# Kernel tuning notes

Hardware: AMD Instinct MI355X
Metric: run time of the kernel (lower is better)

The kernel has to match this reference:

```python
import jax, jax.numpy as jnp
import numpy as np

DIM = 128          # per-stream channels (init arg `dim`)
C = 2 * DIM        # fused channels
NH = 8             # num_heads
HD = C // NH       # head_dim = 32
K = 3              # kernel_size
DIL = (2, 3)       # dilation list
ND = len(DIL)
SCALE = HD ** -0.5


def setup_inputs() -> dict:
    key = jax.random.key(0)
    ks = jax.random.split(key, 4)
    B, H, W = 4, 80, 80
    rgb = jax.random.normal(ks[0], (B, DIM, H, W), jnp.float32)
    ir = jax.random.normal(ks[1], (B, DIM, H, W), jnp.float32)
    w_qkv = jax.random.normal(ks[2], (3 * C, C), jnp.float32) * (C ** -0.5)
    w_proj = jax.random.normal(ks[3], (C, C), jnp.float32) * (C ** -0.5)
    b_proj = jnp.zeros((C,), jnp.float32)
    return {"rgb": rgb, "ir": ir, "w_qkv": w_qkv, "w_proj": w_proj, "b_proj": b_proj}


def _unfold(x, k, d):
    # nn.Unfold(k, dilation=d, padding=d*(k-1)//2, stride=1) -> [B, c, k*k, H, W]
    B, c, H, W = x.shape
    p = d * (k - 1) // 2
    xp = jnp.pad(x, ((0, 0), (0, 0), (p, p), (p, p)))
    pats = [xp[:, :, i * d:i * d + H, j * d:j * d + W]
            for i in range(k) for j in range(k)]
    return jnp.stack(pats, axis=2)


def _dilate_attention(q, k, v, d):
    # q,k,v: [B, c, H, W] with c = C // ND; attention over k*k dilated neighborhood
    B, c, H, W = q.shape
    h = c // HD
    N = H * W
    qr = q.reshape(B, h, HD, N)                      # [B,h,hd,N]
    ku = _unfold(k, K, d).reshape(B, h, HD, K * K, N)  # [B,h,hd,K2,N]
    vu = _unfold(v, K, d).reshape(B, h, HD, K * K, N)
    attn = jnp.einsum('bhdn,bhdkn->bhnk', qr, ku) * SCALE   # [B,h,N,K2]
    attn = jax.nn.softmax(attn, axis=-1)
    out = jnp.einsum('bhnk,bhdkn->bnhd', attn, vu)          # head-major channels
    return out.reshape(B, H, W, c)


def reference(rgb, ir, w_qkv, w_proj, b_proj):
    y = jnp.concatenate([rgb, ir], axis=1)            # [B, C, H, W]
    B, Cc, H, W = y.shape
    # 1x1 conv qkv, then split channels as [3, num_dilation, C//num_dilation]
    qkv = jnp.einsum('bchw,oc->bohw', y, w_qkv).reshape(B, 3, ND, Cc // ND, H, W)
    outs = [_dilate_attention(qkv[:, 0, i], qkv[:, 1, i], qkv[:, 2, i], DIL[i])
            for i in range(ND)]
    x = jnp.concatenate(outs, axis=-1)                # [B, H, W, C], dilation-major
    x = x @ w_proj.T + b_proj                         # proj Linear(C, C)
    # residual: add rgb to first half of channels, ir to second half
    return x + y.transpose(0, 2, 3, 1)
```

## Files before the change

### kernel.cpp

```cpp
#include <hip/hip_runtime.h>

#define HH 80
#define WW 80
#define NPIX 6400
#define NB 4
#define BN 25600
#define CDIM 256
#define QKVC 768
#define SCALE 0.17677669529663689f

typedef __attribute__((ext_vector_type(8))) short short8;
typedef __attribute__((ext_vector_type(4))) float floatx4;

__device__ __forceinline__ float b2f(ushort u) {
    return __uint_as_float(((uint)u) << 16);
}
__device__ __forceinline__ ushort f2b(float f) {
    uint u = __float_as_uint(f);
    return (ushort)((u + 0x7fffu + ((u >> 16) & 1u)) >> 16);
}
__device__ __forceinline__ void unpack8(uint4 v, float* f) {
    f[0] = __uint_as_float(v.x << 16); f[1] = __uint_as_float(v.x & 0xffff0000u);
    f[2] = __uint_as_float(v.y << 16); f[3] = __uint_as_float(v.y & 0xffff0000u);
    f[4] = __uint_as_float(v.z << 16); f[5] = __uint_as_float(v.z & 0xffff0000u);
    f[6] = __uint_as_float(v.w << 16); f[7] = __uint_as_float(v.w & 0xffff0000u);
}
__device__ __forceinline__ void gload_lds16(const void* gptr, void* lptr) {
    __builtin_amdgcn_global_load_lds(
        (const __attribute__((address_space(1))) unsigned int*)gptr,
        (__attribute__((address_space(3))) unsigned int*)lptr,
        16, 0, 0);
}

__global__ __launch_bounds__(256) void cast_all_k(
    const float* __restrict__ rgb, const float* __restrict__ ir,
    const float* __restrict__ wq, const float* __restrict__ wp,
    ushort* __restrict__ Yb, ushort* __restrict__ wqb, ushort* __restrict__ wpb)
{
    const int tid = threadIdx.x;
    if (blockIdx.x >= 100) {
        int i = (((blockIdx.x - 100) * 8 + blockIdx.y) * 4 + blockIdx.z) * 256 + tid;
        if (i < QKVC * CDIM) wqb[i] = f2b(wq[i]);
        else                 wpb[i - QKVC * CDIM] = f2b(wp[i - QKVC * CDIM]);
        return;
    }
    __shared__ ushort T[32][72];
    const int pix0 = blockIdx.x * 64;
    const int cb = blockIdx.y;
    const int b = blockIdx.z;

    const int pl = tid & 63, cg = tid >> 6;
    #pragma unroll
    for (int cc = 0; cc < 32; cc += 4) {
        int c = cb * 32 + cc + cg;
        const float* src = (c < 128) ? (rgb + ((size_t)b * 128 + c) * NPIX)
                                     : (ir + ((size_t)b * 128 + (c - 128)) * NPIX);
        T[cc + cg][pl] = f2b(src[pix0 + pl]);
    }
    __syncthreads();
    const int nl = tid >> 2, c0 = (tid & 3) * 8;
    ushort tmp[8];
    #pragma unroll
    for (int j = 0; j < 8; ++j) tmp[j] = T[c0 + j][nl];
    uint4 v;
    v.x = tmp[0] | ((uint)tmp[1] << 16);
    v.y = tmp[2] | ((uint)tmp[3] << 16);
    v.z = tmp[4] | ((uint)tmp[5] << 16);
    v.w = tmp[6] | ((uint)tmp[7] << 16);
    *(uint4*)(&Yb[((size_t)(b * NPIX + pix0 + nl)) * CDIM + cb * 32 + c0]) = v;
}

__device__ __forceinline__ void gemm_nt_body(
    const ushort* __restrict__ A, const ushort* __restrict__ W,
    ushort* As, ushort* Bs, int n0, int o0, floatx4 acc[4][4])
{
    const int tid = threadIdx.x;
    const int lane = tid & 63;
    const int wave = tid >> 6;
    const int wr = wave >> 1, wc = wave & 1;
    const int l15 = lane & 15, quad = lane >> 4;

    const int srow = tid >> 2;
    const int sk   = (tid & 3) * 8;

    for (int k0 = 0; k0 < CDIM; k0 += 32) {
        #pragma unroll
        for (int p = 0; p < 2; ++p) {
            gload_lds16(&A[(size_t)(n0 + p * 64 + srow) * CDIM + k0 + sk],
                        As + wave * 512 + p * 2048);
            gload_lds16(&W[(size_t)(o0 + p * 64 + srow) * CDIM + k0 + sk],
                        Bs + wave * 512 + p * 2048);
        }
        __syncthreads();
        short8 af[4], bfr[4];
        #pragma unroll
        for (int i = 0; i < 4; ++i)
            af[i] = *(const short8*)(&As[(wr * 64 + i * 16 + l15) * 32 + quad * 8]);
        #pragma unroll
        for (int j = 0; j < 4; ++j)
            bfr[j] = *(const short8*)(&Bs[(wc * 64 + j * 16 + l15) * 32 + quad * 8]);
        #pragma unroll
        for (int i = 0; i < 4; ++i)
            #pragma unroll
            for (int j = 0; j < 4; ++j)
                acc[i][j] = __builtin_amdgcn_mfma_f32_16x16x32_bf16(
                    af[i], bfr[j], acc[i][j], 0, 0, 0);
        __syncthreads();
    }
}

__global__ __launch_bounds__(256) void gemm_qkv_mfma(
    const ushort* __restrict__ Yb, const ushort* __restrict__ Wb,
    ushort* __restrict__ qkv2)
{
    __shared__ __align__(16) ushort As[128 * 32];
    __shared__ __align__(16) ushort Bs[128 * 32];
    const int tid = threadIdx.x;
    const int lane = tid & 63;
    const int wave = tid >> 6;
    const int wr = wave >> 1, wc = wave & 1;
    const int l15 = lane & 15, quad = lane >> 4;
    const int n0 = blockIdx.x * 128;
    const int o0 = blockIdx.y * 128;

    floatx4 acc[4][4] = {};
    gemm_nt_body(Yb, Wb, As, Bs, n0, o0, acc);

    #pragma unroll
    for (int i = 0; i < 4; ++i)
        #pragma unroll
        for (int j = 0; j < 4; ++j) {
            const int o = o0 + wc * 64 + j * 16 + l15;
            ushort* cbase = qkv2 + (size_t)(o >> 5) * BN * 32 + (o & 31);
            #pragma unroll
            for (int r = 0; r < 4; ++r) {
                int n = n0 + wr * 64 + i * 16 + quad * 4 + r;
                cbase[(size_t)n * 32] = f2b(acc[i][j][r]);
            }
        }
}

template<int D>
__device__ __forceinline__ void attn_tile(
    const ushort* __restrict__ qkv2, ushort* __restrict__ X2,
    ushort* kl, int b, int dh, int y0, int x0)
{
    constexpr int RW = 16 + 2 * D;
    constexpr int RP = RW * RW;
    const int tid = threadIdx.x;
    const int lane = tid & 63;
    const int wave = tid >> 6;
    const ushort* Qc = qkv2 + (size_t)dh * BN * 32;
    const ushort* Kc = qkv2 + (size_t)(8 + dh) * BN * 32;
    const ushort* Vc = qkv2 + (size_t)(16 + dh) * BN * 32;

    const int px = tid & 15, py = tid >> 4;
    const int n = b * NPIX + (y0 + py) * WW + (x0 + px);
    float q[32];
    {
        const uint4* qp = (const uint4*)(Qc + (size_t)n * 32);
        uint4 v0 = qp[0], v1 = qp[1], v2 = qp[2], v3 = qp[3];
        unpack8(v0, q); unpack8(v1, q + 8); unpack8(v2, q + 16); unpack8(v3, q + 24);
    }

    for (int p0 = 0; p0 < RP; p0 += 64) {
        int p = p0 + lane;
        int ry = p / RW, rx = p % RW;
        int gy = min(max(y0 - D + ry, 0), HH - 1);
        int gx = min(max(x0 - D + rx, 0), WW - 1);
        if (p < RP)
            gload_lds16(Kc + (size_t)(b * NPIX + gy * WW + gx) * 32 + wave * 8,
                        kl + (size_t)(wave * RP + p0) * 8);
    }
    __syncthreads();

    float sc[9];
    #pragma unroll
    for (int t = 0; t < 9; ++t) {
        const int dy = t / 3 - 1, dx = t % 3 - 1;
        const int yy = y0 + py + dy * D, xx = x0 + px + dx * D;
        const int p = (py + D + dy * D) * RW + (px + D + dx * D);
        float s = 0.f;
        if (yy >= 0 && yy < HH && xx >= 0 && xx < WW) {
            #pragma unroll
            for (int c = 0; c < 4; ++c) {
                float kv[8];
                unpack8(*(const uint4*)(kl + (size_t)(c * RP + p) * 8), kv);
                #pragma unroll
                for (int j = 0; j < 8; ++j) s += q[c * 8 + j] * kv[j];
            }
        }
        sc[t] = s * SCALE;
    }
    float m = sc[0];
    #pragma unroll
    for (int t = 1; t < 9; ++t) m = fmaxf(m, sc[t]);
    float sum = 0.f;
    #pragma unroll
    for (int t = 0; t < 9; ++t) { sc[t] = __expf(sc[t] - m); sum += sc[t]; }
    const float inv = 1.f / sum;

    __syncthreads();
    for (int p0 = 0; p0 < RP; p0 += 64) {
        int p = p0 + lane;
        int ry = p / RW, rx = p % RW;
        int gy = min(max(y0 - D + ry, 0), HH - 1);
        int gx = min(max(x0 - D + rx, 0), WW - 1);
        if (p < RP)
            gload_lds16(Vc + (size_t)(b * NPIX + gy * WW + gx) * 32 + wave * 8,
                        kl + (size_t)(wave * RP + p0) * 8);
    }
    __syncthreads();

    float o[32];
    #pragma unroll
    for (int hd = 0; hd < 32; ++hd) o[hd] = 0.f;
    #pragma unroll
    for (int t = 0; t < 9; ++t) {
        const int dy = t / 3 - 1, dx = t % 3 - 1;
        const int yy = y0 + py + dy * D, xx = x0 + px + dx * D;
        const int p = (py + D + dy * D) * RW + (px + D + dx * D);
        if (yy >= 0 && yy < HH && xx >= 0 && xx < WW) {
            const float wgt = sc[t] * inv;
            #pragma unroll
            for (int c = 0; c < 4; ++c) {
                float vv[8];
                unpack8(*(const uint4*)(kl + (size_t)(c * RP + p) * 8), vv);
                #pragma unroll
                for (int j = 0; j < 8; ++j) o[c * 8 + j] += wgt * vv[j];
            }
        }
    }
    uint4* xp = (uint4*)(X2 + (size_t)dh * BN * 32 + (size_t)n * 32);
    #pragma unroll
    for (int m4 = 0; m4 < 4; ++m4) {
        uint4 v;
        v.x = f2b(o[8 * m4 + 0]) | ((uint)f2b(o[8 * m4 + 1]) << 16);
        v.y = f2b(o[8 * m4 + 2]) | ((uint)f2b(o[8 * m4 + 3]) << 16);
        v.z = f2b(o[8 * m4 + 4]) | ((uint)f2b(o[8 * m4 + 5]) << 16);
        v.w = f2b(o[8 * m4 + 6]) | ((uint)f2b(o[8 * m4 + 7]) << 16);
        xp[m4] = v;
    }
}

__global__ __launch_bounds__(256) void attn2_k(
    const ushort* __restrict__ qkv2, ushort* __restrict__ X2)
{
    __shared__ __align__(16) ushort kl[4 * 484 * 8];
    const int tile = blockIdx.x;
    const int y0 = (tile / 5) * 16, x0 = (tile % 5) * 16;
    const int dh = blockIdx.y;
    const int b = blockIdx.z;
    if (dh < 4) attn_tile<2>(qkv2, X2, kl, b, dh, y0, x0);
    else        attn_tile<3>(qkv2, X2, kl, b, dh, y0, x0);
}

__global__ __launch_bounds__(256) void proj_mfma(
    const ushort* __restrict__ X2, const ushort* __restrict__ Wpb,
    const float* __restrict__ bp, const ushort* __restrict__ Yb,
    float* __restrict__ out)
{
    __shared__ __align__(16) ushort As[128 * 32];
    __shared__ __align__(16) ushort Bs[128 * 32];
    const int tid = threadIdx.x;
    const int lane = tid & 63;
    const int wave = tid >> 6;
    const int wr = wave >> 1, wc = wave & 1;
    const int l15 = lane & 15, quad = lane >> 4;
    const int n0 = blockIdx.x * 128;
    const int o0 = blockIdx.y * 128;

    const int srow = tid >> 2;
    const int sk   = (tid & 3) * 8;

    floatx4 acc[4][4] = {};

    for (int k0 = 0; k0 < CDIM; k0 += 32) {
        const ushort* Achunk = X2 + (size_t)(k0 >> 5) * BN * 32;
        #pragma unroll
        for (int p = 0; p < 2; ++p) {
            gload_lds16(&Achunk[(size_t)(n0 + p * 64 + srow) * 32 + sk],
                        As + wave * 512 + p * 2048);
            gload_lds16(&Wpb[(size_t)(o0 + p * 64 + srow) * CDIM + k0 + sk],
                        Bs + wave * 512 + p * 2048);
        }
        __syncthreads();
        short8 af[4], bfr[4];
        #pragma unroll
        for (int i = 0; i < 4; ++i)
            af[i] = *(const short8*)(&As[(wr * 64 + i * 16 + l15) * 32 + quad * 8]);
        #pragma unroll
        for (int j = 0; j < 4; ++j)
            bfr[j] = *(const short8*)(&Bs[(wc * 64 + j * 16 + l15) * 32 + quad * 8]);
        #pragma unroll
        for (int i = 0; i < 4; ++i)
            #pragma unroll
            for (int j = 0; j < 4; ++j)
                acc[i][j] = __builtin_amdgcn_mfma_f32_16x16x32_bf16(
                    af[i], bfr[j], acc[i][j], 0, 0, 0);
        __syncthreads();
    }

    #pragma unroll
    for (int i = 0; i < 4; ++i)
        #pragma unroll
        for (int j = 0; j < 4; ++j) {
            int o = o0 + wc * 64 + j * 16 + l15;
            float bias = bp[o];
            #pragma unroll
            for (int r = 0; r < 4; ++r) {
                int n = n0 + wr * 64 + i * 16 + quad * 4 + r;
                out[(size_t)n * CDIM + o] =
                    acc[i][j][r] + bias + b2f(Yb[(size_t)n * CDIM + o]);
            }
        }
}

extern "C" void kernel_launch(void* const* d_in, const int* in_sizes, int n_in,
                              void* d_out, int out_size, void* d_ws, size_t ws_size,
                              hipStream_t stream) {
    const float* rgb    = (const float*)d_in[0];
    const float* ir     = (const float*)d_in[1];
    const float* w_qkv  = (const float*)d_in[2];
    const float* w_proj = (const float*)d_in[3];
    const float* b_proj = (const float*)d_in[4];
    float* out = (float*)d_out;

    ushort* qkv2 = (ushort*)d_ws;
    ushort* Yb   = qkv2 + (size_t)24 * BN * 32;
    ushort* X2   = Yb + (size_t)BN * CDIM;
    ushort* Wqb  = X2 + (size_t)8 * BN * 32;
    ushort* Wpb  = Wqb + (size_t)QKVC * CDIM;

    cast_all_k<<<dim3(132, 8, NB), 256, 0, stream>>>(rgb, ir, w_qkv, w_proj,
                                                     Yb, Wqb, Wpb);
    gemm_qkv_mfma<<<dim3(BN / 128, QKVC / 128), 256, 0, stream>>>(Yb, Wqb, qkv2);
    attn2_k<<<dim3(25, 8, NB), 256, 0, stream>>>(qkv2, X2);
    proj_mfma<<<dim3(BN / 128, CDIM / 128), 256, 0, stream>>>(X2, Wpb, b_proj, Yb, out);
}
```

Baseline: 140.0 us.

## Vectorize GEMM epilogues via swapped MFMA operands and specialize interior attention tiles

Swaps the MFMA A/B operands so each lane holds four consecutive output channels for one pixel. The qkv GEMM can then store packed 8-byte bf16 pairs, and the projection can write float4 outputs with vector bias and residual loads, replacing scattered 2-byte and 4-byte stores. Attention tiles that sit fully inside the image get a template variant without clamping or bounds checks. The V-tile load is now issued before the softmax math so the load can overlap it. This adds more code paths and template instantiations, which may raise register pressure.

```diff
diff --git a/kernel.cpp b/kernel.cpp
--- a/kernel.cpp
+++ b/kernel.cpp
@@ -104,7 +104,7 @@
             #pragma unroll
             for (int j = 0; j < 4; ++j)
                 acc[i][j] = __builtin_amdgcn_mfma_f32_16x16x32_bf16(
-                    af[i], bfr[j], acc[i][j], 0, 0, 0);
+                    bfr[j], af[i], acc[i][j], 0, 0, 0);
         __syncthreads();
     }
 }
@@ -127,20 +127,20 @@
     gemm_nt_body(Yb, Wb, As, Bs, n0, o0, acc);
 
     #pragma unroll
-    for (int i = 0; i < 4; ++i)
+    for (int i = 0; i < 4; ++i) {
+        const int n = n0 + wr * 64 + i * 16 + l15;
         #pragma unroll
         for (int j = 0; j < 4; ++j) {
-            const int o = o0 + wc * 64 + j * 16 + l15;
-            ushort* cbase = qkv2 + (size_t)(o >> 5) * BN * 32 + (o & 31);
-            #pragma unroll
-            for (int r = 0; r < 4; ++r) {
-                int n = n0 + wr * 64 + i * 16 + quad * 4 + r;
-                cbase[(size_t)n * 32] = f2b(acc[i][j][r]);
-            }
-        }
-}
-
-template<int D>
+            const int o4 = o0 + wc * 64 + j * 16 + quad * 4;
+            uint2 v;
+            v.x = f2b(acc[i][j][0]) | ((uint)f2b(acc[i][j][1]) << 16);
+            v.y = f2b(acc[i][j][2]) | ((uint)f2b(acc[i][j][3]) << 16);
+            *(uint2*)(qkv2 + (size_t)(o4 >> 5) * BN * 32 + (size_t)n * 32 + (o4 & 31)) = v;
+        }
+    }
+}
+
+template<int D, bool EDGE>
 __device__ __forceinline__ void attn_tile(
     const ushort* __restrict__ qkv2, ushort* __restrict__ X2,
     ushort* kl, int b, int dh, int y0, int x0)
@@ -163,11 +163,12 @@
         unpack8(v0, q); unpack8(v1, q + 8); unpack8(v2, q + 16); unpack8(v3, q + 24);
     }
 
+    #pragma unroll 2
     for (int p0 = 0; p0 < RP; p0 += 64) {
         int p = p0 + lane;
         int ry = p / RW, rx = p % RW;
-        int gy = min(max(y0 - D + ry, 0), HH - 1);
-        int gx = min(max(x0 - D + rx, 0), WW - 1);
+        int gy = y0 - D + ry, gx = x0 - D + rx;
+        if (EDGE) { gy = min(max(gy, 0), HH - 1); gx = min(max(gx, 0), WW - 1); }
         if (p < RP)
             gload_lds16(Kc + (size_t)(b * NPIX + gy * WW + gx) * 32 + wave * 8,
                         kl + (size_t)(wave * RP + p0) * 8);
@@ -178,10 +179,14 @@
     #pragma unroll
     for (int t = 0; t < 9; ++t) {
         const int dy = t / 3 - 1, dx = t % 3 - 1;
-        const int yy = y0 + py + dy * D, xx = x0 + px + dx * D;
         const int p = (py + D + dy * D) * RW + (px + D + dx * D);
         float s = 0.f;
-        if (yy >= 0 && yy < HH && xx >= 0 && xx < WW) {
+        bool ok = true;
+        if (EDGE) {
+            const int yy = y0 + py + dy * D, xx = x0 + px + dx * D;
+            ok = (yy >= 0 && yy < HH && xx >= 0 && xx < WW);
+        }
+        if (ok) {
             #pragma unroll
             for (int c = 0; c < 4; ++c) {
                 float kv[8];
@@ -192,24 +197,26 @@
         }
         sc[t] = s * SCALE;
     }
-    float m = sc[0];
-    #pragma unroll
-    for (int t = 1; t < 9; ++t) m = fmaxf(m, sc[t]);
-    float sum = 0.f;
-    #pragma unroll
-    for (int t = 0; t < 9; ++t) { sc[t] = __expf(sc[t] - m); sum += sc[t]; }
-    const float inv = 1.f / sum;
-
     __syncthreads();
+
+    #pragma unroll 2
     for (int p0 = 0; p0 < RP; p0 += 64) {
         int p = p0 + lane;
         int ry = p / RW, rx = p % RW;
-        int gy = min(max(y0 - D + ry, 0), HH - 1);
-        int gx = min(max(x0 - D + rx, 0), WW - 1);
+        int gy = y0 - D + ry, gx = x0 - D + rx;
+        if (EDGE) { gy = min(max(gy, 0), HH - 1); gx = min(max(gx, 0), WW - 1); }
         if (p < RP)
             gload_lds16(Vc + (size_t)(b * NPIX + gy * WW + gx) * 32 + wave * 8,
                         kl + (size_t)(wave * RP + p0) * 8);
     }
+
+    float m = sc[0];
+    #pragma unroll
+    for (int t = 1; t < 9; ++t) m = fmaxf(m, sc[t]);
+    float sum = 0.f;
+    #pragma unroll
+    for (int t = 0; t < 9; ++t) { sc[t] = __expf(sc[t] - m); sum += sc[t]; }
+    const float inv = 1.f / sum;
     __syncthreads();
 
     float o[32];
@@ -218,9 +225,13 @@
     #pragma unroll
     for (int t = 0; t < 9; ++t) {
         const int dy = t / 3 - 1, dx = t % 3 - 1;
-        const int yy = y0 + py + dy * D, xx = x0 + px + dx * D;
         const int p = (py + D + dy * D) * RW + (px + D + dx * D);
-        if (yy >= 0 && yy < HH && xx >= 0 && xx < WW) {
+        bool ok = true;
+        if (EDGE) {
+            const int yy = y0 + py + dy * D, xx = x0 + px + dx * D;
+            ok = (yy >= 0 && yy < HH && xx >= 0 && xx < WW);
+        }
+        if (ok) {
             const float wgt = sc[t] * inv;
             #pragma unroll
             for (int c = 0; c < 4; ++c) {
@@ -251,8 +262,14 @@
     const int y0 = (tile / 5) * 16, x0 = (tile % 5) * 16;
     const int dh = blockIdx.y;
     const int b = blockIdx.z;
-    if (dh < 4) attn_tile<2>(qkv2, X2, kl, b, dh, y0, x0);
-    else        attn_tile<3>(qkv2, X2, kl, b, dh, y0, x0);
+    const bool inter = (y0 >= 16 && y0 <= 48 && x0 >= 16 && x0 <= 48);
+    if (dh < 4) {
+        if (inter) attn_tile<2, false>(qkv2, X2, kl, b, dh, y0, x0);
+        else       attn_tile<2, true >(qkv2, X2, kl, b, dh, y0, x0);
+    } else {
+        if (inter) attn_tile<3, false>(qkv2, X2, kl, b, dh, y0, x0);
+        else       attn_tile<3, true >(qkv2, X2, kl, b, dh, y0, x0);
+    }
 }
 
 __global__ __launch_bounds__(256) void proj_mfma(
@@ -297,23 +314,26 @@
             #pragma unroll
             for (int j = 0; j < 4; ++j)
                 acc[i][j] = __builtin_amdgcn_mfma_f32_16x16x32_bf16(
-                    af[i], bfr[j], acc[i][j], 0, 0, 0);
+                    bfr[j], af[i], acc[i][j], 0, 0, 0);
         __syncthreads();
     }
 
     #pragma unroll
-    for (int i = 0; i < 4; ++i)
+    for (int i = 0; i < 4; ++i) {
+        const int n = n0 + wr * 64 + i * 16 + l15;
         #pragma unroll
         for (int j = 0; j < 4; ++j) {
-            int o = o0 + wc * 64 + j * 16 + l15;
-            float bias = bp[o];
-            #pragma unroll
-            for (int r = 0; r < 4; ++r) {
-                int n = n0 + wr * 64 + i * 16 + quad * 4 + r;
-                out[(size_t)n * CDIM + o] =
-                    acc[i][j][r] + bias + b2f(Yb[(size_t)n * CDIM + o]);
-            }
-        }
+            const int o4 = o0 + wc * 64 + j * 16 + quad * 4;
+            const float4 bias = *(const float4*)(bp + o4);
+            const ushort4 res = *(const ushort4*)(Yb + (size_t)n * CDIM + o4);
+            float4 v;
+            v.x = acc[i][j][0] + bias.x + b2f(res.x);
+            v.y = acc[i][j][1] + bias.y + b2f(res.y);
+            v.z = acc[i][j][2] + bias.z + b2f(res.z);
+            v.w = acc[i][j][3] + bias.w + b2f(res.w);
+            *(float4*)(out + (size_t)n * CDIM + o4) = v;
+        }
+    }
 }
 
 extern "C" void kernel_launch(void* const* d_in, const int* in_sizes, int n_in,
```

New measurement: 136.0 us. -2.8%, faster.
